# Kernel tuning notes

Hardware: AMD Instinct MI355X
Metric: run time of the kernel (lower is better)

Reference implementation:

```python
import jax, jax.numpy as jnp
import numpy as np

B, L, C, H = 1024, 64, 1024, 16  # windows*batch, window area, dim, heads
D = C // H  # head_dim = 64
WIN = 64  # window_size[0]; window_size = (64, 1)


def _relative_position_index():
    coords = np.arange(WIN)
    idx = coords[:, None] - coords[None, :] + (WIN - 1)
    return jnp.asarray(idx, dtype=jnp.int32)  # [L, L]


def setup_inputs() -> dict:
    key = jax.random.key(0)
    ks = jax.random.split(key, 8)
    s = 0.02
    return {
        "hidden_states": jax.random.normal(ks[0], (B, L, C), dtype=jnp.float32),
        "Wq": jax.random.normal(ks[1], (C, C), dtype=jnp.float32) * s,
        "bq": jax.random.normal(ks[2], (C,), dtype=jnp.float32) * s,
        "Wk": jax.random.normal(ks[3], (C, C), dtype=jnp.float32) * s,
        "bk": jax.random.normal(ks[4], (C,), dtype=jnp.float32) * s,
        "Wv": jax.random.normal(ks[5], (C, C), dtype=jnp.float32) * s,
        "bv": jax.random.normal(ks[6], (C,), dtype=jnp.float32) * s,
        "bias_table": jax.random.normal(ks[7], (2 * WIN - 1, H), dtype=jnp.float32) * s,
        "rel_index": _relative_position_index(),
    }


def reference(hidden_states, Wq, bq, Wk, bk, Wv, bv, bias_table, rel_index):
    b, l, c = hidden_states.shape
    # QKV projections -> [b, H, l, D]
    q = (hidden_states @ Wq + bq).reshape(b, l, H, D).transpose(0, 2, 1, 3)
    k = (hidden_states @ Wk + bk).reshape(b, l, H, D).transpose(0, 2, 1, 3)
    v = (hidden_states @ Wv + bv).reshape(b, l, H, D).transpose(0, 2, 1, 3)
    scores = jnp.einsum("bhqd,bhkd->bhqk", q, k) / jnp.sqrt(jnp.float32(D))
    # relative position bias: gather [L, L, H] -> [1, H, L, L]
    rel_bias = bias_table[rel_index]  # [L, L, H]
    scores = scores + rel_bias.transpose(2, 0, 1)[None]
    probs = jax.nn.softmax(scores, axis=-1)  # dropout p=0.0 (eval)
    context = jnp.einsum("bhqk,bhkd->bhqd", probs, v)
    context = context.transpose(0, 2, 1, 3).reshape(b, l, c)
    return context
```

## Files before the change

### kernel.cpp

```cpp
#include <hip/hip_runtime.h>
#include <hip/hip_fp16.h>
#include <stdint.h>

typedef _Float16 f16;
typedef _Float16 f16x8 __attribute__((ext_vector_type(8)));
typedef _Float16 f16x4 __attribute__((ext_vector_type(4)));
typedef float f32x4 __attribute__((ext_vector_type(4)));

__device__ __forceinline__ void gload_lds16(const void* g, void* l) {
    __builtin_amdgcn_global_load_lds(
        (const __attribute__((address_space(1))) void*)g,
        (__attribute__((address_space(3))) void*)l,
        16, 0, 0);
}

__global__ __launch_bounds__(256) void convert_x(const float* __restrict__ X,
                                                 f16* __restrict__ Xh) {
    size_t i = ((size_t)blockIdx.x * 256 + threadIdx.x) * 8;
    float4 a = *(const float4*)(X + i);
    float4 b = *(const float4*)(X + i + 4);
    f16x8 o;
    o[0] = (f16)a.x; o[1] = (f16)a.y; o[2] = (f16)a.z; o[3] = (f16)a.w;
    o[4] = (f16)b.x; o[5] = (f16)b.y; o[6] = (f16)b.z; o[7] = (f16)b.w;
    *(f16x8*)(Xh + i) = o;
}

__global__ __launch_bounds__(1024) void transpose_w(const float* __restrict__ Wq,
                                                    const float* __restrict__ Wk,
                                                    const float* __restrict__ Wv,
                                                    f16* __restrict__ Wt) {
    __shared__ float tile[32][33];
    const int w = blockIdx.z;
    const float* W = (w == 0) ? Wq : ((w == 1) ? Wk : Wv);
    const int n0 = blockIdx.x * 32, k0 = blockIdx.y * 32;
    const int tx = threadIdx.x, ty = threadIdx.y;
    tile[ty][tx] = W[(size_t)(k0 + ty) * 1024 + n0 + tx];
    __syncthreads();
    Wt[(size_t)(w * 1024 + n0 + ty) * 1024 + k0 + tx] = (f16)tile[tx][ty];
}

__global__ __launch_bounds__(256) void qkv_gemm(const f16* __restrict__ A,
                                                const f16* __restrict__ Bt,
                                                const float* __restrict__ bq,
                                                const float* __restrict__ bk,
                                                const float* __restrict__ bv,
                                                f16* __restrict__ Out) {
    __shared__ __align__(16) f16 sA[128][32];
    __shared__ __align__(16) f16 sB[128][32];

    const int tid  = threadIdx.x;
    const int wave = tid >> 6, lane = tid & 63;
    const int quad = lane >> 4, l16 = lane & 15;
    const int m0 = blockIdx.y * 128, n0 = blockIdx.x * 128;
    const int wm = (wave & 1) * 64, wn = (wave >> 1) * 64;

    const int srow = lane >> 2;
    const int scol = (lane & 3) * 8;
    const f16* gA = A  + (size_t)(m0 + wave * 32 + srow) * 1024 + scol;
    const f16* gB = Bt + (size_t)(n0 + wave * 32 + srow) * 1024 + scol;
    f16* lA = &sA[wave * 32][0];
    f16* lB = &sB[wave * 32][0];

    f32x4 acc[4][4] = {};

    for (int k0 = 0; k0 < 1024; k0 += 32) {
        gload_lds16(gA + k0,             lA);
        gload_lds16(gA + k0 + 16 * 1024, lA + 16 * 32);
        gload_lds16(gB + k0,             lB);
        gload_lds16(gB + k0 + 16 * 1024, lB + 16 * 32);
        __syncthreads();

        f16x8 af[4], bf[4];
#pragma unroll
        for (int t = 0; t < 4; ++t)
            af[t] = *(const f16x8*)&sA[wm + t * 16 + l16][quad * 8];
#pragma unroll
        for (int t = 0; t < 4; ++t)
            bf[t] = *(const f16x8*)&sB[wn + t * 16 + l16][quad * 8];

#pragma unroll
        for (int mt = 0; mt < 4; ++mt)
#pragma unroll
            for (int nt = 0; nt < 4; ++nt)
                acc[mt][nt] = __builtin_amdgcn_mfma_f32_16x16x32_f16(
                    af[mt], bf[nt], acc[mt][nt], 0, 0, 0);
        __syncthreads();
    }

    const int w_idx = n0 >> 10;
    const float* bias = (w_idx == 0) ? bq : ((w_idx == 1) ? bk : bv);
    f16* out = Out + (size_t)w_idx * (65536UL * 1024UL);
    if (w_idx == 2) {
#pragma unroll
        for (int mt = 0; mt < 4; ++mt) {
            const int mb = m0 + wm + mt * 16 + quad * 4;
            const int b = mb >> 6, l0 = mb & 63;
#pragma unroll
            for (int nt = 0; nt < 4; ++nt) {
                const int n  = n0 + wn + nt * 16 + l16;
                const int nc = n & 1023;
                const int hh = nc >> 6, d = nc & 63;
                f16x4 pk;
#pragma unroll
                for (int r = 0; r < 4; ++r)
                    pk[r] = (f16)(acc[mt][nt][r] + bias[nc]);
                *(f16x4*)&out[(((size_t)b * 16 + hh) * 64 + d) * 64 + l0] = pk;
            }
        }
    } else {
#pragma unroll
        for (int mt = 0; mt < 4; ++mt) {
#pragma unroll
            for (int r = 0; r < 4; ++r) {
                const int m = m0 + wm + mt * 16 + quad * 4 + r;
                const int b = m >> 6, l = m & 63;
#pragma unroll
                for (int nt = 0; nt < 4; ++nt) {
                    const int n  = n0 + wn + nt * 16 + l16;
                    const int nc = n & 1023;
                    const int hh = nc >> 6, d = nc & 63;
                    const float v = acc[mt][nt][r] + bias[nc];
                    out[(((size_t)b * 16 + hh) * 64 + l) * 64 + d] = (f16)v;
                }
            }
        }
    }
}

__global__ __launch_bounds__(256) void attn(const f16* __restrict__ QKV,
                                            const float* __restrict__ bias_table,
                                            float* __restrict__ outp) {
    __shared__ __align__(16) f16 sQ[64][72];
    __shared__ __align__(16) f16 sK[64][72];
    __shared__ __align__(16) f16 sVt[64][72];
    __shared__ __align__(16) f16 sP[64][72];
    __shared__ float sBias[128];

    const int bh = blockIdx.x;
    const int h  = bh & 15;
    const int tid  = threadIdx.x;
    const int wave = tid >> 6, lane = tid & 63;
    const int quad = lane >> 4, l16 = lane & 15;

    const f16* Qg = QKV + (size_t)bh * 4096;
    const f16* Kg = Qg + 67108864UL;
    const f16* Vg = Kg + 67108864UL;

    if (tid < 127) sBias[tid] = bias_table[tid * 16 + h];

#pragma unroll
    for (int j = 0; j < 2; ++j) {
        const int idx = tid + j * 256;
        const int e = idx * 8;
        const int r0 = e >> 6, c0 = e & 63;
        *(f16x8*)&sQ[r0][c0]  = *(const f16x8*)(Qg + e);
        *(f16x8*)&sK[r0][c0]  = *(const f16x8*)(Kg + e);
        *(f16x8*)&sVt[r0][c0] = *(const f16x8*)(Vg + e);
    }
    __syncthreads();

    const int ib = wave * 16 + quad * 4;
    float inv[4];

    {
        f32x4 acc[4] = {};
#pragma unroll
        for (int k0 = 0; k0 < 64; k0 += 32) {
            f16x8 a = *(const f16x8*)&sQ[wave * 16 + l16][k0 + quad * 8];
#pragma unroll
            for (int nt = 0; nt < 4; ++nt) {
                f16x8 b = *(const f16x8*)&sK[nt * 16 + l16][k0 + quad * 8];
                acc[nt] = __builtin_amdgcn_mfma_f32_16x16x32_f16(a, b, acc[nt], 0, 0, 0);
            }
        }
        float sv[4][4];
        float mx[4] = {-1e30f, -1e30f, -1e30f, -1e30f};
#pragma unroll
        for (int nt = 0; nt < 4; ++nt) {
            const int j = nt * 16 + l16;
#pragma unroll
            for (int r = 0; r < 4; ++r) {
                const float s = acc[nt][r] * 0.125f + sBias[ib + r - j + 63];
                sv[nt][r] = s;
                mx[r] = fmaxf(mx[r], s);
            }
        }
#pragma unroll
        for (int off = 1; off < 16; off <<= 1)
#pragma unroll
            for (int r = 0; r < 4; ++r)
                mx[r] = fmaxf(mx[r], __shfl_xor(mx[r], off));
        float sum[4] = {0.f, 0.f, 0.f, 0.f};
#pragma unroll
        for (int nt = 0; nt < 4; ++nt)
#pragma unroll
            for (int r = 0; r < 4; ++r) {
                const float e = __expf(sv[nt][r] - mx[r]);
                sv[nt][r] = e;
                sum[r] += e;
            }
#pragma unroll
        for (int off = 1; off < 16; off <<= 1)
#pragma unroll
            for (int r = 0; r < 4; ++r)
                sum[r] += __shfl_xor(sum[r], off);
#pragma unroll
        for (int r = 0; r < 4; ++r) inv[r] = 1.0f / sum[r];
#pragma unroll
        for (int nt = 0; nt < 4; ++nt)
#pragma unroll
            for (int r = 0; r < 4; ++r)
                sP[ib + r][nt * 16 + l16] = (f16)sv[nt][r];
    }
    __syncthreads();

    {
        f32x4 acc[4] = {};
#pragma unroll
        for (int k0 = 0; k0 < 64; k0 += 32) {
            f16x8 a = *(const f16x8*)&sP[wave * 16 + l16][k0 + quad * 8];
#pragma unroll
            for (int nt = 0; nt < 4; ++nt) {
                f16x8 b = *(const f16x8*)&sVt[nt * 16 + l16][k0 + quad * 8];
                acc[nt] = __builtin_amdgcn_mfma_f32_16x16x32_f16(a, b, acc[nt], 0, 0, 0);
            }
        }
        const int b = bh >> 4;
        float* op = outp + ((size_t)b * 64 + ib) * 1024 + h * 64;
#pragma unroll
        for (int nt = 0; nt < 4; ++nt) {
            const int d = nt * 16 + l16;
#pragma unroll
            for (int r = 0; r < 4; ++r)
                op[(size_t)r * 1024 + d] = acc[nt][r] * inv[r];
        }
    }
}

extern "C" void kernel_launch(void* const* d_in, const int* in_sizes, int n_in,
                              void* d_out, int out_size, void* d_ws, size_t ws_size,
                              hipStream_t stream) {
    const float* X          = (const float*)d_in[0];
    const float* Wq         = (const float*)d_in[1];
    const float* bq         = (const float*)d_in[2];
    const float* Wk         = (const float*)d_in[3];
    const float* bk         = (const float*)d_in[4];
    const float* Wv         = (const float*)d_in[5];
    const float* bv         = (const float*)d_in[6];
    const float* bias_table = (const float*)d_in[7];
    float* out = (float*)d_out;

    f16* Xh  = (f16*)d_ws;
    f16* Wt  = Xh + 67108864UL;
    f16* QKV = Wt + 3145728UL;

    convert_x<<<32768, 256, 0, stream>>>(X, Xh);
    transpose_w<<<dim3(32, 32, 3), dim3(32, 32), 0, stream>>>(Wq, Wk, Wv, Wt);
    qkv_gemm<<<dim3(24, 512), 256, 0, stream>>>(Xh, Wt, bq, bk, bv, QKV);
    attn<<<16384, 256, 0, stream>>>(QKV, bias_table, out);
}
```

Measured before the change: 1.071 ms.

## Rewrite QKV GEMM with 256x256 tiles, double-buffered LDS and phased MFMA scheduling

Replaces the 128x128 tile QKV GEMM with a 256x256 tile, 512-thread version that uses a 64-wide K step, XOR-swizzled LDS layout, double-buffered global-to-LDS staging interleaved with MFMA phases, explicit barriers/waitcnt and setprio, and a block-index swizzle for L2 reuse. It aims to cut global/LDS traffic per FLOP and overlap loads with matrix math in the dominant GEMM. It needs 128KB of dynamic LDS (set via function attribute) and many accumulator registers, which limits occupancy.

```diff
diff --git a/kernel.cpp b/kernel.cpp
--- a/kernel.cpp
+++ b/kernel.cpp
@@ -39,92 +39,180 @@
     Wt[(size_t)(w * 1024 + n0 + ty) * 1024 + k0 + tx] = (f16)tile[tx][ty];
 }
 
-__global__ __launch_bounds__(256) void qkv_gemm(const f16* __restrict__ A,
-                                                const f16* __restrict__ Bt,
-                                                const float* __restrict__ bq,
-                                                const float* __restrict__ bk,
-                                                const float* __restrict__ bv,
-                                                f16* __restrict__ Out) {
-    __shared__ __align__(16) f16 sA[128][32];
-    __shared__ __align__(16) f16 sB[128][32];
+__global__ __launch_bounds__(512, 2) void qkv_gemm(const f16* __restrict__ A,
+                                                   const f16* __restrict__ Bt,
+                                                   const float* __restrict__ bq,
+                                                   const float* __restrict__ bk,
+                                                   const float* __restrict__ bv,
+                                                   f16* __restrict__ Out) {
+    extern __shared__ __align__(16) f16 lds[];
 
     const int tid  = threadIdx.x;
     const int wave = tid >> 6, lane = tid & 63;
     const int quad = lane >> 4, l16 = lane & 15;
-    const int m0 = blockIdx.y * 128, n0 = blockIdx.x * 128;
-    const int wm = (wave & 1) * 64, wn = (wave >> 1) * 64;
-
-    const int srow = lane >> 2;
-    const int scol = (lane & 3) * 8;
-    const f16* gA = A  + (size_t)(m0 + wave * 32 + srow) * 1024 + scol;
-    const f16* gB = Bt + (size_t)(n0 + wave * 32 + srow) * 1024 + scol;
-    f16* lA = &sA[wave * 32][0];
-    f16* lB = &sB[wave * 32][0];
-
-    f32x4 acc[4][4] = {};
-
-    for (int k0 = 0; k0 < 1024; k0 += 32) {
-        gload_lds16(gA + k0,             lA);
-        gload_lds16(gA + k0 + 16 * 1024, lA + 16 * 32);
-        gload_lds16(gB + k0,             lB);
-        gload_lds16(gB + k0 + 16 * 1024, lB + 16 * 32);
-        __syncthreads();
-
-        f16x8 af[4], bf[4];
-#pragma unroll
-        for (int t = 0; t < 4; ++t)
-            af[t] = *(const f16x8*)&sA[wm + t * 16 + l16][quad * 8];
-#pragma unroll
-        for (int t = 0; t < 4; ++t)
-            bf[t] = *(const f16x8*)&sB[wn + t * 16 + l16][quad * 8];
-
-#pragma unroll
-        for (int mt = 0; mt < 4; ++mt)
-#pragma unroll
-            for (int nt = 0; nt < 4; ++nt)
-                acc[mt][nt] = __builtin_amdgcn_mfma_f32_16x16x32_f16(
-                    af[mt], bf[nt], acc[mt][nt], 0, 0, 0);
-        __syncthreads();
+    const int wm = wave >> 2, wn = wave & 3;
+
+    const int bid = blockIdx.x;
+    const int swz = (bid & 7) * 384 + (bid >> 3);
+    const int m0 = (swz & 255) * 256;
+    const int n0 = (swz >> 8) * 256;
+
+    const int sub  = lane >> 3;
+    const int swzc = (lane & 7) ^ sub;
+    const int stDst = wave * 512 + lane * 8;
+    const f16* gA0 = A  + (size_t)(m0 + wave * 8 + sub) * 1024 + swzc * 8;
+    const f16* gB0 = Bt + (size_t)(n0 + wave * 8 + sub) * 1024 + swzc * 8;
+
+#define STAGE_A(D, H, KT) do {                                                  \
+        const f16* _g = gA0 + (H) * 65536 + (KT) * 64;                          \
+        gload_lds16(_g,          &lds[(D) * 16384 + (H) * 8192 + stDst]);       \
+        gload_lds16(_g + 131072, &lds[(D) * 16384 + (H) * 8192 + 4096 + stDst]);\
+    } while (0)
+#define STAGE_B(D, H, KT) do {                                                  \
+        const f16* _g = gB0 + (H) * 131072 + (KT) * 64;                         \
+        gload_lds16(_g,         &lds[32768 + (D) * 16384 + (H) * 8192 + stDst]);\
+        gload_lds16(_g + 65536, &lds[32768 + (D) * 16384 + (H) * 8192 + 4096 + stDst]); \
+    } while (0)
+
+    const int l7  = l16 & 7;
+    const int cA0 = ((0 + quad) ^ l7) * 8;
+    const int cA1 = ((4 + quad) ^ l7) * 8;
+    const int aRow = (wm * 64 + l16) * 64;
+    int bOff[4];
+#pragma unroll
+    for (int nf = 0; nf < 4; ++nf) {
+        const int pr = wn * 64 + nf * 16 + l16;
+        bOff[nf] = (pr >> 7) * 8192 + (pr & 127) * 64;
+    }
+
+    f32x4 acc[8][4] = {};
+    f16x8 bf[4][2];
+
+#define LOAD_A(G, V0, V1)                                                        \
+    f16x8 V0 = *(const f16x8*)&lds[aIdx + ((G) >> 2) * 8192 + ((G)&3) * 1024 + cA0]; \
+    f16x8 V1 = *(const f16x8*)&lds[aIdx + ((G) >> 2) * 8192 + ((G)&3) * 1024 + cA1];
+
+#define MFMA_PAIR(G0, G1)                                                        \
+    _Pragma("unroll")                                                            \
+    for (int nf = 0; nf < 4; ++nf) {                                             \
+        acc[G0][nf] = __builtin_amdgcn_mfma_f32_16x16x32_f16(aA0, bf[nf][0], acc[G0][nf], 0, 0, 0); \
+        acc[G0][nf] = __builtin_amdgcn_mfma_f32_16x16x32_f16(aA1, bf[nf][1], acc[G0][nf], 0, 0, 0); \
+        acc[G1][nf] = __builtin_amdgcn_mfma_f32_16x16x32_f16(aB0, bf[nf][0], acc[G1][nf], 0, 0, 0); \
+        acc[G1][nf] = __builtin_amdgcn_mfma_f32_16x16x32_f16(aB1, bf[nf][1], acc[G1][nf], 0, 0, 0); \
+    }
+
+#define PHASE_MID()                                        \
+    __builtin_amdgcn_sched_barrier(0);                     \
+    __builtin_amdgcn_s_barrier();                          \
+    asm volatile("s_waitcnt lgkmcnt(0)" ::: "memory");     \
+    __builtin_amdgcn_sched_barrier(0);                     \
+    __builtin_amdgcn_s_setprio(1);
+
+#define PHASE_END()                                        \
+    __builtin_amdgcn_s_setprio(0);                         \
+    __builtin_amdgcn_sched_barrier(0);                     \
+    __builtin_amdgcn_s_barrier();
+
+#define PHASE_END_WAIT(N)                                  \
+    __builtin_amdgcn_s_setprio(0);                         \
+    __builtin_amdgcn_sched_barrier(0);                     \
+    asm volatile("s_waitcnt vmcnt(" #N ")" ::: "memory");  \
+    __builtin_amdgcn_s_barrier();
+
+    STAGE_B(0, 0, 0); STAGE_B(0, 1, 0); STAGE_A(0, 0, 0); STAGE_A(0, 1, 0);
+    STAGE_B(1, 0, 1); STAGE_B(1, 1, 1); STAGE_A(1, 0, 1);
+    asm volatile("s_waitcnt vmcnt(6)" ::: "memory");
+    __builtin_amdgcn_s_barrier();
+
+    for (int t = 0; t < 16; ++t) {
+        const int d    = t & 1;
+        const int aIdx = d * 16384 + aRow;
+        const int bIdx = 32768 + d * 16384;
+
+        {
+#pragma unroll
+            for (int nf = 0; nf < 4; ++nf) {
+                bf[nf][0] = *(const f16x8*)&lds[bIdx + bOff[nf] + cA0];
+                bf[nf][1] = *(const f16x8*)&lds[bIdx + bOff[nf] + cA1];
+            }
+            LOAD_A(0, aA0, aA1); LOAD_A(1, aB0, aB1);
+            if (t + 1 < 16) STAGE_A(d ^ 1, 1, t + 1);
+            PHASE_MID();
+            MFMA_PAIR(0, 1);
+            PHASE_END();
+        }
+        {
+            LOAD_A(2, aA0, aA1); LOAD_A(3, aB0, aB1);
+            if (t + 2 < 16) STAGE_B(d, 0, t + 2);
+            PHASE_MID();
+            MFMA_PAIR(2, 3);
+            PHASE_END();
+        }
+        {
+            LOAD_A(4, aA0, aA1); LOAD_A(5, aB0, aB1);
+            if (t + 2 < 16) STAGE_B(d, 1, t + 2);
+            PHASE_MID();
+            MFMA_PAIR(4, 5);
+            PHASE_END();
+        }
+        {
+            LOAD_A(6, aA0, aA1); LOAD_A(7, aB0, aB1);
+            if (t + 2 < 16) STAGE_A(d, 0, t + 2);
+            PHASE_MID();
+            MFMA_PAIR(6, 7);
+            if (t < 14) {
+                PHASE_END_WAIT(6);
+            } else if (t == 14) {
+                PHASE_END_WAIT(0);
+            } else {
+                PHASE_END();
+            }
+        }
     }
 
     const int w_idx = n0 >> 10;
     const float* bias = (w_idx == 0) ? bq : ((w_idx == 1) ? bk : bv);
-    f16* out = Out + (size_t)w_idx * (65536UL * 1024UL);
+    f16* outp = Out + (size_t)w_idx * 67108864UL;
     if (w_idx == 2) {
 #pragma unroll
-        for (int mt = 0; mt < 4; ++mt) {
-            const int mb = m0 + wm + mt * 16 + quad * 4;
+        for (int mg = 0; mg < 8; ++mg) {
+            const int mb = m0 + wm * 128 + mg * 16 + quad * 4;
             const int b = mb >> 6, l0 = mb & 63;
 #pragma unroll
-            for (int nt = 0; nt < 4; ++nt) {
-                const int n  = n0 + wn + nt * 16 + l16;
-                const int nc = n & 1023;
-                const int hh = nc >> 6, d = nc & 63;
+            for (int nf = 0; nf < 4; ++nf) {
+                const int nc = (n0 + wn * 64 + nf * 16 + l16) & 1023;
+                const int hh = nc >> 6, dd = nc & 63;
                 f16x4 pk;
 #pragma unroll
                 for (int r = 0; r < 4; ++r)
-                    pk[r] = (f16)(acc[mt][nt][r] + bias[nc]);
-                *(f16x4*)&out[(((size_t)b * 16 + hh) * 64 + d) * 64 + l0] = pk;
+                    pk[r] = (f16)(acc[mg][nf][r] + bias[nc]);
+                *(f16x4*)&outp[(((size_t)b * 16 + hh) * 64 + dd) * 64 + l0] = pk;
             }
         }
     } else {
 #pragma unroll
-        for (int mt = 0; mt < 4; ++mt) {
+        for (int mg = 0; mg < 8; ++mg) {
 #pragma unroll
             for (int r = 0; r < 4; ++r) {
-                const int m = m0 + wm + mt * 16 + quad * 4 + r;
+                const int m = m0 + wm * 128 + mg * 16 + quad * 4 + r;
                 const int b = m >> 6, l = m & 63;
 #pragma unroll
-                for (int nt = 0; nt < 4; ++nt) {
-                    const int n  = n0 + wn + nt * 16 + l16;
-                    const int nc = n & 1023;
-                    const int hh = nc >> 6, d = nc & 63;
-                    const float v = acc[mt][nt][r] + bias[nc];
-                    out[(((size_t)b * 16 + hh) * 64 + l) * 64 + d] = (f16)v;
+                for (int nf = 0; nf < 4; ++nf) {
+                    const int nc = (n0 + wn * 64 + nf * 16 + l16) & 1023;
+                    const int hh = nc >> 6, dd = nc & 63;
+                    const float v = acc[mg][nf][r] + bias[nc];
+                    outp[(((size_t)b * 16 + hh) * 64 + l) * 64 + dd] = (f16)v;
                 }
             }
         }
     }
+#undef STAGE_A
+#undef STAGE_B
+#undef LOAD_A
+#undef MFMA_PAIR
+#undef PHASE_MID
+#undef PHASE_END
+#undef PHASE_END_WAIT
 }
 
 __global__ __launch_bounds__(256) void attn(const f16* __restrict__ QKV,
@@ -254,8 +342,15 @@
     f16* Wt  = Xh + 67108864UL;
     f16* QKV = Wt + 3145728UL;
 
+    static bool lds_cfg = false;
+    if (!lds_cfg) {
+        hipFuncSetAttribute((const void*)qkv_gemm,
+                            hipFuncAttributeMaxDynamicSharedMemorySize, 131072);
+        lds_cfg = true;
+    }
+
     convert_x<<<32768, 256, 0, stream>>>(X, Xh);
     transpose_w<<<dim3(32, 32, 3), dim3(32, 32), 0, stream>>>(Wq, Wk, Wv, Wt);
-    qkv_gemm<<<dim3(24, 512), 256, 0, stream>>>(Xh, Wt, bq, bk, bv, QKV);
+    qkv_gemm<<<3072, 512, 131072, stream>>>(Xh, Wt, bq, bk, bv, QKV);
     attn<<<16384, 256, 0, stream>>>(QKV, bias_table, out);
 }
```

Result: faster. 990.4 us (-7.5%).
